# Kernel tuning notes

Measured on AMD Instinct MI355X. Metric: run time of the kernel, lower is better.

## Reference

```python
import jax, jax.numpy as jnp
import numpy as np

B, C, D, H, EXP = 4, 1024, 1024, 16, 4
EPS = 1e-6


def ffn_layernorm(x, w, b):
    # normalize over channel axis (dim 1); w,b have shape (1, C)
    u = jnp.mean(x, axis=1, keepdims=True)
    s = jnp.mean((x - u) ** 2, axis=1, keepdims=True)
    xn = (x - u) / jnp.sqrt(s + EPS)
    return w[:, :, None] * xn + b[:, :, None]


def softmax_one(x):
    # exp(x - max) / (1 + sum exp(x - max)), exactly as the torch SoftmaxOne
    m = jnp.max(x, axis=-1, keepdims=True)
    e = jnp.exp(x - m)
    return e / (1.0 + jnp.sum(e, axis=-1, keepdims=True))


def setup_inputs() -> dict:
    key = jax.random.key(0)
    ks = jax.random.split(key, 20)
    n = lambda k, shape, s=0.02: jax.random.normal(k, shape, dtype=jnp.float32) * s
    inp = {
        "x1": jax.random.normal(ks[0], (B, C, D), dtype=jnp.float32),
        "lnq_w": jnp.ones((1, C), jnp.float32) + n(ks[1], (1, C)),
        "lnq_b": n(ks[2], (1, C)),
        "lnk_w": jnp.ones((1, C), jnp.float32) + n(ks[3], (1, C)),
        "lnk_b": n(ks[4], (1, C)),
        "lnv_w": jnp.ones((1, C), jnp.float32) + n(ks[5], (1, C)),
        "lnv_b": n(ks[6], (1, C)),
        "wq": n(ks[7], (D, D)),
        "bq": n(ks[8], (D,)),
        "wk": n(ks[9], (D, D)),
        "bk": n(ks[10], (D,)),
        "wv": n(ks[11], (D, D)),
        "bv": n(ks[12], (D,)),
        "ffnln_w": jnp.ones((1, C), jnp.float32) + n(ks[13], (1, C)),
        "ffnln_b": n(ks[14], (1, C)),
        "conv1_w": n(ks[15], (C * EXP, C)),
        "conv1_b": n(ks[16], (C * EXP,)),
        "conv2_w": n(ks[17], (C, C * EXP)),
        "conv2_b": n(ks[18], (C,)),
    }
    return inp


def reference(x1, lnq_w, lnq_b, lnk_w, lnk_b, lnv_w, lnv_b,
              wq, bq, wk, bk, wv, bv,
              ffnln_w, ffnln_b, conv1_w, conv1_b, conv2_w, conv2_b):
    b, c, d = x1.shape
    dh = d // H
    q = ffn_layernorm(x1, lnq_w, lnq_b)
    k = ffn_layernorm(x1, lnk_w, lnk_b)
    v = ffn_layernorm(x1, lnv_w, lnv_b)
    # nn.Linear: y = x @ W.T + b, then the torch code's direct reshape
    # (b, c, d) -> (b, H, c, dh) (NOT a transpose-split)
    q = (q @ wq.T + bq).reshape(b, H, c, dh)
    k = (k @ wk.T + bk).reshape(b, H, c, dh)
    v = (v @ wv.T + bv).reshape(b, H, c, dh)
    scale = 1.0 / np.sqrt(dh).astype(np.float32)
    attn = jnp.einsum("bhqe,bhke->bhqk", q * scale, k)
    attn_weights = softmax_one(attn)
    o = jnp.einsum("bhqk,bhke->bhqe", attn_weights, v)
    o = o.transpose(0, 2, 1, 3).reshape(b, c, d)
    x = x1 + o
    # FFN: channel LayerNorm -> 1x1 conv (channel mix) -> GELU -> 1x1 conv
    xl = ffn_layernorm(x, ffnln_w, ffnln_b)
    h1 = jnp.einsum("oc,bcl->bol", conv1_w, xl) + conv1_b[None, :, None]
    h1 = jax.nn.gelu(h1, approximate=False)
    h2 = jnp.einsum("oc,bcl->bol", conv2_w, h1) + conv2_b[None, :, None]
    return (x + h2, attn_weights)
```

## Files before the change

kernel.cpp:

```cpp
#include <hip/hip_runtime.h>
#include <hip/hip_bf16.h>
#include <math.h>


typedef __bf16 bf16;
typedef __bf16 bf16x4 __attribute__((ext_vector_type(4)));
typedef __bf16 bf16x8 __attribute__((ext_vector_type(8)));
typedef float floatx4 __attribute__((ext_vector_type(4)));

#define MFMA16(a, b, c) __builtin_amdgcn_mfma_f32_16x16x32_bf16(a, b, c, 0, 0, 0)

__device__ __forceinline__ void gload16(const void* g, void* l) {
    __builtin_amdgcn_global_load_lds((__attribute__((address_space(1))) void*)g,
                                     (__attribute__((address_space(3))) void*)l,
                                     16, 0, 0);
}

__global__ __launch_bounds__(256)
void cast_all(const float* __restrict__ s0, bf16* __restrict__ d0_,
              const float* __restrict__ s1, bf16* __restrict__ d1_,
              const float* __restrict__ s2, bf16* __restrict__ d2_,
              const float* __restrict__ s3, bf16* __restrict__ d3_,
              const float* __restrict__ s4, bf16* __restrict__ d4_)
{
    int blk = blockIdx.x;
    const float* s; bf16* d; int base;
    if (blk < 1024)      { s = s0; d = d0_; base = blk; }
    else if (blk < 2048) { s = s1; d = d1_; base = blk - 1024; }
    else if (blk < 3072) { s = s2; d = d2_; base = blk - 2048; }
    else if (blk < 7168) { s = s3; d = d3_; base = blk - 3072; }
    else                 { s = s4; d = d4_; base = blk - 7168; }
    long i = ((long)base << 10) + (threadIdx.x << 2);
    float4 v = *(const float4*)(s + i);
    bf16x4 o;
    o[0] = (bf16)v.x; o[1] = (bf16)v.y; o[2] = (bf16)v.z; o[3] = (bf16)v.w;
    *(bf16x4*)(d + i) = o;
}

__global__ __launch_bounds__(256)
void stats_part(const float* __restrict__ xin, float* __restrict__ ps,
                float* __restrict__ pq)
{
    __shared__ float S1[4][64];
    __shared__ float S2[4][64];
    const int b = blockIdx.z, chunk = blockIdx.y;
    const int d0 = blockIdx.x << 6;
    const int tid = threadIdx.x;
    const int dl = tid & 63, cg = tid >> 6;
    const float* xp = xin + ((long)b << 20) + d0 + dl;
    const int cbase = (chunk << 8) + (cg << 6);
    float s = 0.f, sq = 0.f;
    for (int c = 0; c < 64; ++c) {
        float v = xp[(long)(cbase + c) << 10];
        s += v; sq += v * v;
    }
    S1[cg][dl] = s; S2[cg][dl] = sq;
    __syncthreads();
    if (tid < 64) {
        float ts = S1[0][tid] + S1[1][tid] + S1[2][tid] + S1[3][tid];
        float tq = S2[0][tid] + S2[1][tid] + S2[2][tid] + S2[3][tid];
        int idx = ((b * 4 + chunk) << 10) + d0 + tid;
        ps[idx] = ts; pq[idx] = tq;
    }
}

__global__ __launch_bounds__(256)
void ln_qkv_kernel(const float* __restrict__ x1, const float* __restrict__ ps,
                   const float* __restrict__ pq,
                   const float* __restrict__ wq, const float* __restrict__ bq,
                   const float* __restrict__ wk, const float* __restrict__ bk,
                   const float* __restrict__ wv, const float* __restrict__ bv,
                   bf16* __restrict__ lnq, bf16* __restrict__ lnk,
                   bf16* __restrict__ lnv)
{
    const int bc = blockIdx.x;
    const int c = bc & 1023, b = bc >> 10;
    const int d = threadIdx.x << 2;
    const long i = ((long)bc << 10) + d;
    const float* pb = ps + (b << 12) + d;
    const float* qb = pq + (b << 12) + d;
    float s0 = 0.f, s1 = 0.f, s2 = 0.f, s3 = 0.f;
    float q0 = 0.f, q1 = 0.f, q2 = 0.f, q3 = 0.f;
#pragma unroll
    for (int c4 = 0; c4 < 4; ++c4) {
        float4 pv = *(const float4*)(pb + (c4 << 10));
        float4 qv = *(const float4*)(qb + (c4 << 10));
        s0 += pv.x; s1 += pv.y; s2 += pv.z; s3 += pv.w;
        q0 += qv.x; q1 += qv.y; q2 += qv.z; q3 += qv.w;
    }
    const float inv1024 = 1.f / 1024.f;
    float u0 = s0 * inv1024, u1 = s1 * inv1024, u2 = s2 * inv1024, u3 = s3 * inv1024;
    float r0 = rsqrtf(q0 * inv1024 - u0 * u0 + 1e-6f);
    float r1 = rsqrtf(q1 * inv1024 - u1 * u1 + 1e-6f);
    float r2 = rsqrtf(q2 * inv1024 - u2 * u2 + 1e-6f);
    float r3 = rsqrtf(q3 * inv1024 - u3 * u3 + 1e-6f);
    const float4 xv = *(const float4*)(x1 + i);
    float xn0 = (xv.x - u0) * r0;
    float xn1 = (xv.y - u1) * r1;
    float xn2 = (xv.z - u2) * r2;
    float xn3 = (xv.w - u3) * r3;
    float sw, sb; bf16x4 o;
    sw = wq[c]; sb = bq[c];
    o[0]=(bf16)(sw*xn0+sb); o[1]=(bf16)(sw*xn1+sb); o[2]=(bf16)(sw*xn2+sb); o[3]=(bf16)(sw*xn3+sb);
    *(bf16x4*)(lnq + i) = o;
    sw = wk[c]; sb = bk[c];
    o[0]=(bf16)(sw*xn0+sb); o[1]=(bf16)(sw*xn1+sb); o[2]=(bf16)(sw*xn2+sb); o[3]=(bf16)(sw*xn3+sb);
    *(bf16x4*)(lnk + i) = o;
    sw = wv[c]; sb = bv[c];
    o[0]=(bf16)(sw*xn0+sb); o[1]=(bf16)(sw*xn1+sb); o[2]=(bf16)(sw*xn2+sb); o[3]=(bf16)(sw*xn3+sb);
    *(bf16x4*)(lnv + i) = o;
}

template<int MODE>
__global__ __launch_bounds__(256, 3)
void gemm_nt(const bf16* __restrict__ Ab, const bf16* __restrict__ Bb,
             void* __restrict__ Outb, float* __restrict__ Part,
             const float* __restrict__ bias0, const float* __restrict__ bias1,
             const float* __restrict__ bias2, const float* __restrict__ residb,
             long sAz, long sBz, long sOz, long sRz, long sPz,
             int M, int N, int K, int Ksub, int zdiv)
{
    __shared__ __align__(16) bf16 As[2][128 * 32];
    __shared__ __align__(16) bf16 Bs[2][128 * 32];
    const int z = blockIdx.z;
    const int zb = z / zdiv, kz = z % zdiv;
    const bf16* A = Ab + (long)zb * sAz + (long)kz * Ksub;
    const bf16* B = Bb + (long)zb * sBz + (long)kz * Ksub;
    const float* bias = (zb == 0) ? bias0 : (zb == 1 ? bias1 : bias2);
    const int m0 = blockIdx.y << 7, n0 = blockIdx.x << 7;
    const int tid = threadIdx.x;
    const int wave = tid >> 6, lane = tid & 63;
    const int wm = (wave & 1) << 6, wn = (wave >> 1) << 6;
    const int lm = lane & 15, quad = lane >> 4;
    const bf16* Ag = A + (long)m0 * K;
    const bf16* Bg = B + (long)n0 * K;

    floatx4 acc[4][4] = {};
    const int nt = Ksub >> 5;

#pragma unroll
    for (int r_ = 0; r_ < 2; ++r_) {
        int s_ = (r_ << 8) + tid;
        int lrow = s_ >> 2;
        long go = (long)lrow * K + ((s_ & 3) << 3);
        gload16(Ag + go, &As[0][s_ << 3]);
        gload16(Bg + go, &Bs[0][s_ << 3]);
    }
    __syncthreads();

    for (int t = 0; t < nt; ++t) {
        const int cur = t & 1;
        if (t + 1 < nt) {
            const int kofs = (t + 1) << 5;
#pragma unroll
            for (int r_ = 0; r_ < 2; ++r_) {
                int s_ = (r_ << 8) + tid;
                int lrow = s_ >> 2;
                long go = (long)lrow * K + kofs + ((s_ & 3) << 3);
                gload16(Ag + go, &As[cur ^ 1][s_ << 3]);
                gload16(Bg + go, &Bs[cur ^ 1][s_ << 3]);
            }
        }
        bf16x8 af[4], bfv[4];
#pragma unroll
        for (int i = 0; i < 4; ++i) {
            af[i]  = *(const bf16x8*)(&As[cur][((wm + i * 16 + lm) << 5) + (quad << 3)]);
            bfv[i] = *(const bf16x8*)(&Bs[cur][((wn + i * 16 + lm) << 5) + (quad << 3)]);
        }
        __builtin_amdgcn_s_setprio(1);
#pragma unroll
        for (int mi = 0; mi < 4; ++mi)
#pragma unroll
            for (int ni = 0; ni < 4; ++ni)
                acc[mi][ni] = MFMA16(af[mi], bfv[ni], acc[mi][ni]);
        __builtin_amdgcn_s_setprio(0);
        __syncthreads();
    }

    const int quad4 = quad << 2;
    if (MODE == 2) {
        if (kz == 0) {
            float* Out = (float*)Outb + (long)zb * sOz;
            const float* R = residb + (long)zb * sRz;
#pragma unroll
            for (int mi = 0; mi < 4; ++mi)
#pragma unroll
                for (int ni = 0; ni < 4; ++ni)
#pragma unroll
                    for (int r = 0; r < 4; ++r) {
                        int row = m0 + wm + mi * 16 + quad4 + r;
                        int col = n0 + wn + ni * 16 + lm;
                        long idx = (long)row * N + col;
                        Out[idx] = acc[mi][ni][r] + bias[row] + R[idx];
                    }
        } else {
            float* Out = Part + (long)zb * sPz;
#pragma unroll
            for (int mi = 0; mi < 4; ++mi)
#pragma unroll
                for (int ni = 0; ni < 4; ++ni)
#pragma unroll
                    for (int r = 0; r < 4; ++r) {
                        int row = m0 + wm + mi * 16 + quad4 + r;
                        int col = n0 + wn + ni * 16 + lm;
                        Out[(long)row * N + col] = acc[mi][ni][r];
                    }
        }
    } else {
        bf16* Out = (bf16*)Outb + (long)zb * sOz;
#pragma unroll
        for (int mi = 0; mi < 4; ++mi)
#pragma unroll
            for (int ni = 0; ni < 4; ++ni)
#pragma unroll
                for (int r = 0; r < 4; ++r) {
                    int row = m0 + wm + mi * 16 + quad4 + r;
                    int col = n0 + wn + ni * 16 + lm;
                    float v = acc[mi][ni][r] + bias[col];
                    if (MODE == 1)
                        v = 0.5f * v * (1.0f + erff(v * 0.70710678118654752f));
                    Out[(long)row * N + col] = (bf16)v;
                }
    }
}

__global__ __launch_bounds__(256)
void addpart(float* __restrict__ out, const float* __restrict__ part)
{
    long i = (((long)blockIdx.x << 8) + threadIdx.x) << 2;
    float4 o = *(const float4*)(out + i);
    float4 p = *(const float4*)(part + i);
    o.x += p.x; o.y += p.y; o.z += p.z; o.w += p.w;
    *(float4*)(out + i) = o;
}

__global__ __launch_bounds__(256)
void vtrans_kernel(const bf16* __restrict__ v, bf16* __restrict__ vt)
{
    __shared__ bf16 T[64][66];
    const int p = blockIdx.y;
    const int k0 = blockIdx.x << 6;
    const bf16* V = v + ((long)p << 16);
    bf16* Vt = vt + ((long)p << 16);
    const int tid = threadIdx.x;
    const int e = tid & 63, g = tid >> 6;
#pragma unroll
    for (int j = 0; j < 16; ++j) {
        int kk = (g << 4) + j;
        T[e][kk] = V[((long)(k0 + kk) << 6) + e];
    }
    __syncthreads();
#pragma unroll
    for (int j = 0; j < 16; ++j) {
        int er = (g << 4) + j;
        Vt[((long)er << 10) + k0 + e] = T[er][e];
    }
}

__global__ __launch_bounds__(256)
void attn_kernel(const bf16* __restrict__ q, const bf16* __restrict__ k,
                 const bf16* __restrict__ vt, const float* __restrict__ x1,
                 float* __restrict__ attw, float* __restrict__ x)
{
    __shared__ __align__(16) bf16 Wl[16][1032];
    __shared__ float red[16][4];
    const int bid = blockIdx.x;
    const int p = ((bid & 7) << 3) | ((bid >> 3) & 7);
    const int s = bid >> 6;
    const int b = p >> 4, h = p & 15;
    const bf16* Qp = q + ((long)b << 20) + ((long)h << 16);
    const bf16* Kp = k + ((long)b << 20) + ((long)h << 16);
    const bf16* Vt = vt + ((long)p << 16);
    const int tid = threadIdx.x, w = tid >> 6, lane = tid & 63;
    const int lm = lane & 15, quad = lane >> 4;
    const int r0 = s << 4, kc0 = w << 8;

    floatx4 acc[16];
#pragma unroll
    for (int t = 0; t < 16; ++t) acc[t] = (floatx4){0.f, 0.f, 0.f, 0.f};

#pragma unroll
    for (int e0 = 0; e0 < 64; e0 += 32) {
        bf16x8 aq = *(const bf16x8*)(Qp + ((long)(r0 + lm) << 6) + e0 + quad * 8);
#pragma unroll
        for (int t = 0; t < 16; ++t) {
            bf16x8 bk = *(const bf16x8*)(Kp + ((long)(kc0 + t * 16 + lm) << 6) + e0 + quad * 8);
            acc[t] = MFMA16(aq, bk, acc[t]);
        }
    }
#pragma unroll
    for (int t = 0; t < 16; ++t)
#pragma unroll
        for (int r = 0; r < 4; ++r) acc[t][r] *= 0.125f;

    float mloc[4];
#pragma unroll
    for (int r = 0; r < 4; ++r) {
        float mm = acc[0][r];
#pragma unroll
        for (int t = 1; t < 16; ++t) mm = fmaxf(mm, acc[t][r]);
        mloc[r] = mm;
    }
#pragma unroll
    for (int off = 1; off < 16; off <<= 1)
#pragma unroll
        for (int r = 0; r < 4; ++r) mloc[r] = fmaxf(mloc[r], __shfl_xor(mloc[r], off, 64));
    if (lm == 0)
#pragma unroll
        for (int r = 0; r < 4; ++r) red[quad * 4 + r][w] = mloc[r];
    __syncthreads();
    float mfin[4];
#pragma unroll
    for (int r = 0; r < 4; ++r) {
        int row = quad * 4 + r;
        mfin[r] = fmaxf(fmaxf(red[row][0], red[row][1]), fmaxf(red[row][2], red[row][3]));
    }
    float sloc[4] = {0.f, 0.f, 0.f, 0.f};
#pragma unroll
    for (int t = 0; t < 16; ++t)
#pragma unroll
        for (int r = 0; r < 4; ++r) {
            float e = __expf(acc[t][r] - mfin[r]);
            acc[t][r] = e;
            sloc[r] += e;
        }
#pragma unroll
    for (int off = 1; off < 16; off <<= 1)
#pragma unroll
        for (int r = 0; r < 4; ++r) sloc[r] += __shfl_xor(sloc[r], off, 64);
    __syncthreads();
    if (lm == 0)
#pragma unroll
        for (int r = 0; r < 4; ++r) red[quad * 4 + r][w] = sloc[r];
    __syncthreads();
    float inv[4];
#pragma unroll
    for (int r = 0; r < 4; ++r) {
        int row = quad * 4 + r;
        inv[r] = 1.f / (1.f + red[row][0] + red[row][1] + red[row][2] + red[row][3]);
    }
#pragma unroll
    for (int r = 0; r < 4; ++r) {
        int row = quad * 4 + r;
        float iv = inv[r];
#pragma unroll
        for (int t = 0; t < 16; ++t)
            Wl[row][kc0 + t * 16 + lm] = (bf16)(acc[t][r] * iv);
    }
    __syncthreads();

    floatx4 opv[4];
#pragma unroll
    for (int ni = 0; ni < 4; ++ni) opv[ni] = (floatx4){0.f, 0.f, 0.f, 0.f};
#pragma unroll
    for (int i = 0; i < 8; ++i) {
        const int kk = kc0 + i * 32;
        bf16x8 a0 = *(const bf16x8*)&Wl[lm][kk + quad * 8];
#pragma unroll
        for (int ni = 0; ni < 4; ++ni) {
            bf16x8 bv = *(const bf16x8*)(Vt + ((long)(ni * 16 + lm) << 10) + kk + quad * 8);
            opv[ni] = MFMA16(a0, bv, opv[ni]);
        }
    }
    {
        float* attp = attw + ((long)p << 20) + ((long)r0 << 10);
#pragma unroll
        for (int i = 0; i < 16; ++i) {
            int v4 = (i << 8) + tid;
            int row = v4 >> 8, col = (v4 & 255) << 2;
            bf16x4 wv = *(const bf16x4*)&Wl[row][col];
            floatx4 o = {(float)wv[0], (float)wv[1], (float)wv[2], (float)wv[3]};
            __builtin_nontemporal_store(o, (floatx4*)(attp + ((long)row << 10) + col));
        }
    }
    __syncthreads();
    float* Ored = (float*)&Wl[0][0];
#pragma unroll
    for (int ni = 0; ni < 4; ++ni)
#pragma unroll
        for (int r = 0; r < 4; ++r)
            Ored[(w * 16 + quad * 4 + r) * 64 + ni * 16 + lm] = opv[ni][r];
    __syncthreads();
    const float* x1p = x1 + ((long)b << 20) + ((long)r0 << 10) + (h << 6);
    float* xp = x + ((long)b << 20) + ((long)r0 << 10) + (h << 6);
#pragma unroll
    for (int j = 0; j < 4; ++j) {
        int el = tid + (j << 8);
        int row = el >> 6, cc = el & 63;
        float o = Ored[row * 64 + cc] + Ored[(16 + row) * 64 + cc]
                + Ored[(32 + row) * 64 + cc] + Ored[(48 + row) * 64 + cc];
        xp[((long)row << 10) + cc] = x1p[((long)row << 10) + cc] + o;
    }
}

__global__ __launch_bounds__(256)
void ln_ffn_t_kernel(const float* __restrict__ x, const float* __restrict__ ps,
                     const float* __restrict__ pq, const float* __restrict__ fw,
                     const float* __restrict__ fb, bf16* __restrict__ xlT)
{
    __shared__ bf16 T[64][66];
    const int b = blockIdx.z;
    const int l0 = blockIdx.x << 6, c0 = blockIdx.y << 6;
    const int tid = threadIdx.x;
    const int ll = tid & 63, g = tid >> 6;
    float s = 0.f, q = 0.f;
#pragma unroll
    for (int c4 = 0; c4 < 4; ++c4) {
        s += ps[(b << 12) + (c4 << 10) + l0 + ll];
        q += pq[(b << 12) + (c4 << 10) + l0 + ll];
    }
    const float uu = s * (1.f / 1024.f);
    const float rr = rsqrtf(q * (1.f / 1024.f) - uu * uu + 1e-6f);
#pragma unroll
    for (int j = 0; j < 16; ++j) {
        int cc = (g << 4) + j;
        float v = x[((long)b << 20) + ((long)(c0 + cc) << 10) + l0 + ll];
        T[ll][cc] = (bf16)(fw[c0 + cc] * (v - uu) * rr + fb[c0 + cc]);
    }
    __syncthreads();
#pragma unroll
    for (int j = 0; j < 16; ++j) {
        int lr = (g << 4) + j;
        xlT[((long)b << 20) + ((long)(l0 + lr) << 10) + c0 + ll] = T[lr][ll];
    }
}

extern "C" void kernel_launch(void* const* d_in, const int* in_sizes, int n_in,
                              void* d_out, int out_size, void* d_ws, size_t ws_size,
                              hipStream_t stream)
{
    const float* x1      = (const float*)d_in[0];
    const float* lnq_w   = (const float*)d_in[1];
    const float* lnq_b   = (const float*)d_in[2];
    const float* lnk_w   = (const float*)d_in[3];
    const float* lnk_b   = (const float*)d_in[4];
    const float* lnv_w   = (const float*)d_in[5];
    const float* lnv_b   = (const float*)d_in[6];
    const float* wq      = (const float*)d_in[7];
    const float* bq      = (const float*)d_in[8];
    const float* wk      = (const float*)d_in[9];
    const float* bk      = (const float*)d_in[10];
    const float* wv      = (const float*)d_in[11];
    const float* bv      = (const float*)d_in[12];
    const float* ffnln_w = (const float*)d_in[13];
    const float* ffnln_b = (const float*)d_in[14];
    const float* conv1_w = (const float*)d_in[15];
    const float* conv1_b = (const float*)d_in[16];
    const float* conv2_w = (const float*)d_in[17];
    const float* conv2_b = (const float*)d_in[18];
    (void)in_sizes; (void)n_in; (void)out_size; (void)ws_size;

    char* ws = (char*)d_ws;
    const size_t OFF_VT   = 262144;
    const size_t OFF_QKV  = OFF_VT   + 8388608;
    const size_t OFF_WQKV = OFF_QKV  + 25165824;
    const size_t OFF_W1   = OFF_WQKV + 8388608;
    const size_t OFF_X    = OFF_W1   + 8388608;
    const size_t OFF_W2   = OFF_X    + 16777216;
    float* ps    = (float*)(ws + 65536);
    float* pq    = (float*)(ws + 131072);
    bf16*  vt    = (bf16*)(ws + OFF_VT);
    bf16*  qkv   = (bf16*)(ws + OFF_QKV);
    bf16*  wqkvb = (bf16*)(ws + OFF_WQKV);
    bf16*  w1b   = (bf16*)(ws + OFF_W1);
    float* x     = (float*)(ws + OFF_X);
    bf16*  w2b   = (bf16*)(ws + OFF_W2);
    bf16*  h1T   = (bf16*)(ws + OFF_VT);
    bf16*  xlT   = (bf16*)(ws + OFF_WQKV);
    float* part  = (float*)(ws + OFF_WQKV);

    float* out0 = (float*)d_out;
    float* attw = (float*)((char*)d_out + 16777216);
    bf16*  lnqkv = (bf16*)attw;

    cast_all<<<11264, 256, 0, stream>>>(wq, wqkvb, wk, wqkvb + (1 << 20),
                                        wv, wqkvb + (2 << 20), conv1_w, w1b, conv2_w, w2b);
    stats_part<<<dim3(16, 4, 4), 256, 0, stream>>>(x1, ps, pq);
    ln_qkv_kernel<<<4096, 256, 0, stream>>>(x1, ps, pq, lnq_w, lnq_b, lnk_w, lnk_b,
                                            lnv_w, lnv_b, lnqkv, lnqkv + (1L << 22),
                                            lnqkv + (2L << 22));
    gemm_nt<0><<<dim3(8, 32, 3), 256, 0, stream>>>(lnqkv, wqkvb, qkv, nullptr, bq, bk, bv,
                                                   nullptr, 1L << 22, 1L << 20, 1L << 22, 0, 0,
                                                   4096, 1024, 1024, 1024, 1);
    vtrans_kernel<<<dim3(16, 64), 256, 0, stream>>>(qkv + (2L << 22), vt);
    attn_kernel<<<4096, 256, 0, stream>>>(qkv, qkv + (1L << 22), vt, x1, attw, x);
    stats_part<<<dim3(16, 4, 4), 256, 0, stream>>>(x, ps, pq);
    ln_ffn_t_kernel<<<dim3(16, 16, 4), 256, 0, stream>>>(x, ps, pq, ffnln_w, ffnln_b, xlT);
    gemm_nt<1><<<dim3(32, 8, 4), 256, 0, stream>>>(xlT, w1b, h1T, nullptr, conv1_b, conv1_b,
                                                   conv1_b, nullptr, 1L << 20, 0, 1L << 22, 0, 0,
                                                   1024, 4096, 1024, 1024, 1);
    gemm_nt<2><<<dim3(8, 8, 8), 256, 0, stream>>>(w2b, h1T, out0, part, conv2_b, conv2_b,
                                                  conv2_b, x, 0, 1L << 22, 1L << 20, 1L << 20,
                                                  1L << 20, 1024, 1024, 4096, 2048, 2);
    addpart<<<4096, 256, 0, stream>>>(out0, part);
}
```

Measured before the change: 622.1 us.

## Fold QKV LayerNorm affine into GEMM epilogue and triple-buffer GEMM loads

The per-projection LayerNorm scale and bias are moved algebraically into the QKV GEMM epilogue. The shared normalized x1 is written once in bf16 instead of three times, and the bias term uses precomputed weight row sums, produced by extra blocks in the cast kernel. The GEMM mainloop changes from double to triple buffering, with explicit vmcnt waits and raw barriers so two tiles are in flight. This cuts the LN write traffic and the QKV read traffic and deepens load latency hiding, at the cost of more LDS per block (which may lower occupancy) and an extra row-sum pass.

```diff
diff --git a/kernel.cpp b/kernel.cpp
--- a/kernel.cpp
+++ b/kernel.cpp
@@ -21,16 +21,38 @@
               const float* __restrict__ s1, bf16* __restrict__ d1_,
               const float* __restrict__ s2, bf16* __restrict__ d2_,
               const float* __restrict__ s3, bf16* __restrict__ d3_,
-              const float* __restrict__ s4, bf16* __restrict__ d4_)
-{
-    int blk = blockIdx.x;
+              const float* __restrict__ s4, bf16* __restrict__ d4_,
+              float* __restrict__ rsumout)
+{
+    __shared__ float S[64][4];
+    const int blk = blockIdx.x;
+    const int tid = threadIdx.x;
+    if (blk >= 11264) {
+        const int j = blk - 11264;
+        const int seg = j >> 4;
+        const int obase = (j & 15) << 6;
+        const float* W = seg == 0 ? s0 : (seg == 1 ? s1 : s2);
+        float* outr = rsumout + (seg << 10);
+        const int lane = tid & 63, wv_ = tid >> 6;
+        for (int oi = 0; oi < 64; ++oi) {
+            const float4 w4 = *(const float4*)(W + ((long)(obase + oi) << 10) + (tid << 2));
+            float p = w4.x + w4.y + w4.z + w4.w;
+#pragma unroll
+            for (int off = 1; off < 64; off <<= 1) p += __shfl_xor(p, off, 64);
+            if (lane == 0) S[oi][wv_] = p;
+        }
+        __syncthreads();
+        if (tid < 64)
+            outr[obase + tid] = S[tid][0] + S[tid][1] + S[tid][2] + S[tid][3];
+        return;
+    }
     const float* s; bf16* d; int base;
     if (blk < 1024)      { s = s0; d = d0_; base = blk; }
     else if (blk < 2048) { s = s1; d = d1_; base = blk - 1024; }
     else if (blk < 3072) { s = s2; d = d2_; base = blk - 2048; }
     else if (blk < 7168) { s = s3; d = d3_; base = blk - 3072; }
     else                 { s = s4; d = d4_; base = blk - 7168; }
-    long i = ((long)base << 10) + (threadIdx.x << 2);
+    long i = ((long)base << 10) + (tid << 2);
     float4 v = *(const float4*)(s + i);
     bf16x4 o;
     o[0] = (bf16)v.x; o[1] = (bf16)v.y; o[2] = (bf16)v.z; o[3] = (bf16)v.w;
@@ -65,16 +87,11 @@
 }
 
 __global__ __launch_bounds__(256)
-void ln_qkv_kernel(const float* __restrict__ x1, const float* __restrict__ ps,
-                   const float* __restrict__ pq,
-                   const float* __restrict__ wq, const float* __restrict__ bq,
-                   const float* __restrict__ wk, const float* __restrict__ bk,
-                   const float* __restrict__ wv, const float* __restrict__ bv,
-                   bf16* __restrict__ lnq, bf16* __restrict__ lnk,
-                   bf16* __restrict__ lnv)
+void ln_x1_kernel(const float* __restrict__ x1, const float* __restrict__ ps,
+                  const float* __restrict__ pq, bf16* __restrict__ xn)
 {
     const int bc = blockIdx.x;
-    const int c = bc & 1023, b = bc >> 10;
+    const int b = bc >> 10;
     const int d = threadIdx.x << 2;
     const long i = ((long)bc << 10) + d;
     const float* pb = ps + (b << 12) + d;
@@ -95,20 +112,12 @@
     float r2 = rsqrtf(q2 * inv1024 - u2 * u2 + 1e-6f);
     float r3 = rsqrtf(q3 * inv1024 - u3 * u3 + 1e-6f);
     const float4 xv = *(const float4*)(x1 + i);
-    float xn0 = (xv.x - u0) * r0;
-    float xn1 = (xv.y - u1) * r1;
-    float xn2 = (xv.z - u2) * r2;
-    float xn3 = (xv.w - u3) * r3;
-    float sw, sb; bf16x4 o;
-    sw = wq[c]; sb = bq[c];
-    o[0]=(bf16)(sw*xn0+sb); o[1]=(bf16)(sw*xn1+sb); o[2]=(bf16)(sw*xn2+sb); o[3]=(bf16)(sw*xn3+sb);
-    *(bf16x4*)(lnq + i) = o;
-    sw = wk[c]; sb = bk[c];
-    o[0]=(bf16)(sw*xn0+sb); o[1]=(bf16)(sw*xn1+sb); o[2]=(bf16)(sw*xn2+sb); o[3]=(bf16)(sw*xn3+sb);
-    *(bf16x4*)(lnk + i) = o;
-    sw = wv[c]; sb = bv[c];
-    o[0]=(bf16)(sw*xn0+sb); o[1]=(bf16)(sw*xn1+sb); o[2]=(bf16)(sw*xn2+sb); o[3]=(bf16)(sw*xn3+sb);
-    *(bf16x4*)(lnv + i) = o;
+    bf16x4 o;
+    o[0] = (bf16)((xv.x - u0) * r0);
+    o[1] = (bf16)((xv.y - u1) * r1);
+    o[2] = (bf16)((xv.z - u2) * r2);
+    o[3] = (bf16)((xv.w - u3) * r3);
+    *(bf16x4*)(xn + i) = o;
 }
 
 template<int MODE>
@@ -117,11 +126,15 @@
              void* __restrict__ Outb, float* __restrict__ Part,
              const float* __restrict__ bias0, const float* __restrict__ bias1,
              const float* __restrict__ bias2, const float* __restrict__ residb,
+             const float* __restrict__ lnw0, const float* __restrict__ lnw1,
+             const float* __restrict__ lnw2,
+             const float* __restrict__ lnbq, const float* __restrict__ lnbk,
+             const float* __restrict__ lnbv, const float* __restrict__ rsum,
              long sAz, long sBz, long sOz, long sRz, long sPz,
              int M, int N, int K, int Ksub, int zdiv)
 {
-    __shared__ __align__(16) bf16 As[2][128 * 32];
-    __shared__ __align__(16) bf16 Bs[2][128 * 32];
+    __shared__ __align__(16) bf16 As[3][128 * 32];
+    __shared__ __align__(16) bf16 Bs[3][128 * 32];
     const int z = blockIdx.z;
     const int zb = z / zdiv, kz = z % zdiv;
     const bf16* A = Ab + (long)zb * sAz + (long)kz * Ksub;
@@ -132,34 +145,31 @@
     const int wave = tid >> 6, lane = tid & 63;
     const int wm = (wave & 1) << 6, wn = (wave >> 1) << 6;
     const int lm = lane & 15, quad = lane >> 4;
-    const bf16* Ag = A + (long)m0 * K;
-    const bf16* Bg = B + (long)n0 * K;
-
+    const long rA0 = (long)(tid >> 2) * K;
+    const long rA1 = (long)((tid >> 2) + 64) * K;
+    const int kc8 = (tid & 3) << 3;
+    const bf16* Ag = A + (long)m0 * K + kc8;
+    const bf16* Bg = B + (long)n0 * K + kc8;
+    const int nt = Ksub >> 5;
     floatx4 acc[4][4] = {};
-    const int nt = Ksub >> 5;
-
-#pragma unroll
-    for (int r_ = 0; r_ < 2; ++r_) {
-        int s_ = (r_ << 8) + tid;
-        int lrow = s_ >> 2;
-        long go = (long)lrow * K + ((s_ & 3) << 3);
-        gload16(Ag + go, &As[0][s_ << 3]);
-        gload16(Bg + go, &Bs[0][s_ << 3]);
-    }
-    __syncthreads();
-
+
+    auto STAGE = [&](int pf_, int kt_) {
+        gload16(Ag + rA0 + kt_, &As[pf_][tid << 3]);
+        gload16(Ag + rA1 + kt_, &As[pf_][(tid + 256) << 3]);
+        gload16(Bg + rA0 + kt_, &Bs[pf_][tid << 3]);
+        gload16(Bg + rA1 + kt_, &Bs[pf_][(tid + 256) << 3]);
+    };
+
+    STAGE(0, 0);
+    STAGE(1, 32);
+    asm volatile("s_waitcnt vmcnt(4)" ::: "memory");
+    __builtin_amdgcn_s_barrier();
+
+    int cur = 0;
     for (int t = 0; t < nt; ++t) {
-        const int cur = t & 1;
-        if (t + 1 < nt) {
-            const int kofs = (t + 1) << 5;
-#pragma unroll
-            for (int r_ = 0; r_ < 2; ++r_) {
-                int s_ = (r_ << 8) + tid;
-                int lrow = s_ >> 2;
-                long go = (long)lrow * K + kofs + ((s_ & 3) << 3);
-                gload16(Ag + go, &As[cur ^ 1][s_ << 3]);
-                gload16(Bg + go, &Bs[cur ^ 1][s_ << 3]);
-            }
+        if (t + 2 < nt) {
+            int pf = cur - 1; if (pf < 0) pf += 3;
+            STAGE(pf, (t + 2) << 5);
         }
         bf16x8 af[4], bfv[4];
 #pragma unroll
@@ -174,7 +184,10 @@
             for (int ni = 0; ni < 4; ++ni)
                 acc[mi][ni] = MFMA16(af[mi], bfv[ni], acc[mi][ni]);
         __builtin_amdgcn_s_setprio(0);
-        __syncthreads();
+        if (t + 2 < nt) asm volatile("s_waitcnt vmcnt(4)" ::: "memory");
+        else            asm volatile("s_waitcnt vmcnt(0)" ::: "memory");
+        __builtin_amdgcn_s_barrier();
+        cur = (cur == 2) ? 0 : cur + 1;
     }
 
     const int quad4 = quad << 2;
@@ -206,6 +219,25 @@
                         Out[(long)row * N + col] = acc[mi][ni][r];
                     }
         }
+    } else if (MODE == 0) {
+        bf16* Out = (bf16*)Outb + (long)zb * sOz;
+        const float* lw = (zb == 0) ? lnw0 : (zb == 1 ? lnw1 : lnw2);
+        const float* lb = (zb == 0) ? lnbq : (zb == 1 ? lnbk : lnbv);
+        const float* rs = rsum + (zb << 10);
+#pragma unroll
+        for (int mi = 0; mi < 4; ++mi)
+#pragma unroll
+            for (int r = 0; r < 4; ++r) {
+                const int row = m0 + wm + mi * 16 + quad4 + r;
+                const int crow = row & 1023;
+                const float lwv = lw[crow], lbv = lb[crow];
+#pragma unroll
+                for (int ni = 0; ni < 4; ++ni) {
+                    int col = n0 + wn + ni * 16 + lm;
+                    float v = lwv * acc[mi][ni][r] + lbv * rs[col] + bias[col];
+                    Out[(long)row * N + col] = (bf16)v;
+                }
+            }
     } else {
         bf16* Out = (bf16*)Outb + (long)zb * sOz;
 #pragma unroll
@@ -217,8 +249,7 @@
                     int row = m0 + wm + mi * 16 + quad4 + r;
                     int col = n0 + wn + ni * 16 + lm;
                     float v = acc[mi][ni][r] + bias[col];
-                    if (MODE == 1)
-                        v = 0.5f * v * (1.0f + erff(v * 0.70710678118654752f));
+                    v = 0.5f * v * (1.0f + erff(v * 0.70710678118654752f));
                     Out[(long)row * N + col] = (bf16)v;
                 }
     }
@@ -457,6 +488,7 @@
     const size_t OFF_W1   = OFF_WQKV + 8388608;
     const size_t OFF_X    = OFF_W1   + 8388608;
     const size_t OFF_W2   = OFF_X    + 16777216;
+    float* rsum  = (float*)(ws + 0);
     float* ps    = (float*)(ws + 65536);
     float* pq    = (float*)(ws + 131072);
     bf16*  vt    = (bf16*)(ws + OFF_VT);
@@ -471,26 +503,34 @@
 
     float* out0 = (float*)d_out;
     float* attw = (float*)((char*)d_out + 16777216);
-    bf16*  lnqkv = (bf16*)attw;
-
-    cast_all<<<11264, 256, 0, stream>>>(wq, wqkvb, wk, wqkvb + (1 << 20),
-                                        wv, wqkvb + (2 << 20), conv1_w, w1b, conv2_w, w2b);
+    bf16*  xn   = (bf16*)attw;
+
+    cast_all<<<11312, 256, 0, stream>>>(wq, wqkvb, wk, wqkvb + (1 << 20),
+                                        wv, wqkvb + (2 << 20), conv1_w, w1b, conv2_w, w2b,
+                                        rsum);
     stats_part<<<dim3(16, 4, 4), 256, 0, stream>>>(x1, ps, pq);
-    ln_qkv_kernel<<<4096, 256, 0, stream>>>(x1, ps, pq, lnq_w, lnq_b, lnk_w, lnk_b,
-                                            lnv_w, lnv_b, lnqkv, lnqkv + (1L << 22),
-                                            lnqkv + (2L << 22));
-    gemm_nt<0><<<dim3(8, 32, 3), 256, 0, stream>>>(lnqkv, wqkvb, qkv, nullptr, bq, bk, bv,
-                                                   nullptr, 1L << 22, 1L << 20, 1L << 22, 0, 0,
+    ln_x1_kernel<<<4096, 256, 0, stream>>>(x1, ps, pq, xn);
+    gemm_nt<0><<<dim3(8, 32, 3), 256, 0, stream>>>(xn, wqkvb, qkv, nullptr,
+                                                   bq, bk, bv, nullptr,
+                                                   lnq_w, lnk_w, lnv_w,
+                                                   lnq_b, lnk_b, lnv_b, rsum,
+                                                   0, 1L << 20, 1L << 22, 0, 0,
                                                    4096, 1024, 1024, 1024, 1);
     vtrans_kernel<<<dim3(16, 64), 256, 0, stream>>>(qkv + (2L << 22), vt);
     attn_kernel<<<4096, 256, 0, stream>>>(qkv, qkv + (1L << 22), vt, x1, attw, x);
     stats_part<<<dim3(16, 4, 4), 256, 0, stream>>>(x, ps, pq);
     ln_ffn_t_kernel<<<dim3(16, 16, 4), 256, 0, stream>>>(x, ps, pq, ffnln_w, ffnln_b, xlT);
-    gemm_nt<1><<<dim3(32, 8, 4), 256, 0, stream>>>(xlT, w1b, h1T, nullptr, conv1_b, conv1_b,
-                                                   conv1_b, nullptr, 1L << 20, 0, 1L << 22, 0, 0,
+    gemm_nt<1><<<dim3(32, 8, 4), 256, 0, stream>>>(xlT, w1b, h1T, nullptr,
+                                                   conv1_b, conv1_b, conv1_b, nullptr,
+                                                   nullptr, nullptr, nullptr,
+                                                   nullptr, nullptr, nullptr, nullptr,
+                                                   1L << 20, 0, 1L << 22, 0, 0,
                                                    1024, 4096, 1024, 1024, 1);
-    gemm_nt<2><<<dim3(8, 8, 8), 256, 0, stream>>>(w2b, h1T, out0, part, conv2_b, conv2_b,
-                                                  conv2_b, x, 0, 1L << 22, 1L << 20, 1L << 20,
+    gemm_nt<2><<<dim3(8, 8, 8), 256, 0, stream>>>(w2b, h1T, out0, part,
+                                                  conv2_b, conv2_b, conv2_b, x,
+                                                  nullptr, nullptr, nullptr,
+                                                  nullptr, nullptr, nullptr, nullptr,
+                                                  0, 1L << 22, 1L << 20, 1L << 20,
                                                   1L << 20, 1024, 1024, 4096, 2048, 2);
     addpart<<<4096, 256, 0, stream>>>(out0, part);
 }
```

After: 657.9 us. 1.06x slower.
